# Kernel optimization log

Hardware: AMD Instinct MI355X
Metric: run time of the kernel (lower is better)

Reference implementation:

```python
import jax, jax.numpy as jnp
import numpy as np

N_NODES = 100000
N_EDGES = 1000000
D_NODE = 64
D_EDGE = 32
D_OUT = 64
EPS = 1e-07
BETA = 1.0


def setup_inputs() -> dict:
    key = jax.random.key(0)
    ks = jax.random.split(key, 6)
    node_feats = jax.random.normal(ks[0], (N_NODES, D_NODE), dtype=jnp.float32)
    edge_feats = jax.random.normal(ks[1], (N_EDGES, D_EDGE), dtype=jnp.float32)
    src = jax.random.randint(ks[2], (N_EDGES,), 0, N_NODES, dtype=jnp.int32)
    dst = jax.random.randint(ks[3], (N_EDGES,), 0, N_NODES, dtype=jnp.int32)
    We = jax.random.normal(ks[4], (D_EDGE, D_OUT), dtype=jnp.float32) / np.sqrt(D_EDGE)
    be = jnp.zeros((D_OUT,), dtype=jnp.float32)
    Wm = jax.random.normal(ks[5], (D_NODE, D_OUT), dtype=jnp.float32) / np.sqrt(D_NODE)
    bm = jnp.zeros((D_OUT,), dtype=jnp.float32)
    return {"node_feats": node_feats, "edge_feats": edge_feats, "src": src,
            "dst": dst, "We": We, "be": be, "Wm": Wm, "bm": bm}


def reference(node_feats, edge_feats, src, dst, We, be, Wm, bm):
    n = node_feats.shape[0]
    # edge encoder + u_add_e: m_e = h_src + Linear(e)
    m = node_feats[src] + (edge_feats @ We + be)          # [E, D]
    m = jax.nn.relu(m) + EPS
    # segmented (per-destination) softmax over edges, per feature channel
    z = m * BETA
    zmax = jax.ops.segment_max(z, dst, num_segments=n)    # [N, D]
    ez = jnp.exp(z - zmax[dst])                           # [E, D]
    denom = jax.ops.segment_sum(ez, dst, num_segments=n)  # [N, D]
    a = ez / denom[dst]                                   # [E, D]
    # weighted scatter-sum aggregation
    agg = jax.ops.segment_sum(m * a, dst, num_segments=n) # [N, D]
    feats = node_feats + agg
    # mlp_layers=1 -> single Linear
    return feats @ Wm + bm
```

## Files before the change

### kernel.cpp

```cpp
#include <hip/hip_runtime.h>

#define D_NODE 64
#define D_EDGE 32
#define D_OUT  64
#define EPSF   1e-7f
#define CAP    48
#define CHUNK  8

typedef const __attribute__((address_space(1))) unsigned int guint_t;
typedef __attribute__((address_space(3))) unsigned int luint_t;

__global__ __launch_bounds__(256) void genconv_build_kernel(
    const int* __restrict__ src,
    const int* __restrict__ dst,
    int* __restrict__ cnt,
    int2* __restrict__ slots,
    int E)
{
    const int e = blockIdx.x * blockDim.x + threadIdx.x;
    if (e >= E) return;
    const int d = dst[e];
    const int pos = atomicAdd(&cnt[d], 1);
    if (pos < CAP)
        slots[d * CAP + pos] = make_int2(e, src[e]);
}

__global__ __launch_bounds__(256) void genconv_gather_kernel(
    const float* __restrict__ node,
    const float* __restrict__ ef,
    const int*  __restrict__ cnt,
    const int2* __restrict__ slots,
    const float* __restrict__ We,
    const float* __restrict__ be,
    const float* __restrict__ Wm,
    const float* __restrict__ bm,
    float* __restrict__ out,
    int N)
{
    __shared__ float wm_s[D_NODE * D_OUT];
    __shared__ __align__(16) float efs[4][2][CHUNK * D_EDGE];
    __shared__ __align__(16) float fbuf[4][D_NODE];

    for (int i = threadIdx.x; i < D_NODE * D_OUT; i += blockDim.x)
        wm_s[i] = Wm[i];
    __syncthreads();

    const int lane  = (int)(threadIdx.x & 63);
    const int wslot = (int)(threadIdx.x >> 6);
    float* const efA = efs[wslot][0];
    float* const efB = efs[wslot][1];

    float w[D_EDGE];
#pragma unroll
    for (int k = 0; k < D_EDGE; ++k)
        w[k] = We[k * D_OUT + lane];
    const float bias_e = be[lane];
    const float bias_m = bm[lane];

    const int wid = (int)((blockIdx.x * blockDim.x + threadIdx.x) >> 6);
    const int nw  = (int)((gridDim.x * blockDim.x) >> 6);

    int n = wid;
    int   c_pf   = 0;
    int2  sl_pf  = make_int2(0, 0);
    float res_pf = 0.0f;
    if (n < N) {
        c_pf   = cnt[n];
        sl_pf  = (lane < CAP) ? slots[n * CAP + lane] : make_int2(0, 0);
        res_pf = node[(size_t)n * D_NODE + lane];
    }

    struct HB { float h0, h1, h2, h3, h4, h5, h6, h7; };

    while (n < N) {
        const int c = min(c_pf, CAP);
        const int e_l = (lane < c) ? sl_pf.x : 0;
        const int s_l = (lane < c) ? sl_pf.y : 0;
        const float fres = res_pf;

        const int n_next = n + nw;
        if (n_next < N) {
            c_pf   = cnt[n_next];
            sl_pf  = (lane < CAP) ? slots[n_next * CAP + lane] : make_int2(0, 0);
            res_pf = node[(size_t)n_next * D_NODE + lane];
        }
        __builtin_amdgcn_sched_barrier(0);

        float num = 0.0f, den = 0.0f;

        auto stage = [&](int base, float* dstLDS) {
            const int r  = base + (lane >> 3);
            const int er = __builtin_amdgcn_ds_bpermute(r << 2, e_l);
            const float* g = ef + (size_t)er * D_EDGE + ((lane & 7) << 2);
            __builtin_amdgcn_global_load_lds((guint_t*)g, (luint_t*)dstLDS, 16, 0, 0);
        };
        auto hload = [&](int base, HB& H) {
            const int s0 = __builtin_amdgcn_readlane(s_l, base + 0);
            const int s1 = __builtin_amdgcn_readlane(s_l, base + 1);
            const int s2 = __builtin_amdgcn_readlane(s_l, base + 2);
            const int s3 = __builtin_amdgcn_readlane(s_l, base + 3);
            const int s4 = __builtin_amdgcn_readlane(s_l, base + 4);
            const int s5 = __builtin_amdgcn_readlane(s_l, base + 5);
            const int s6 = __builtin_amdgcn_readlane(s_l, base + 6);
            const int s7 = __builtin_amdgcn_readlane(s_l, base + 7);
            H.h0 = node[(size_t)s0 * D_NODE + lane];
            H.h1 = node[(size_t)s1 * D_NODE + lane];
            H.h2 = node[(size_t)s2 * D_NODE + lane];
            H.h3 = node[(size_t)s3 * D_NODE + lane];
            H.h4 = node[(size_t)s4 * D_NODE + lane];
            H.h5 = node[(size_t)s5 * D_NODE + lane];
            H.h6 = node[(size_t)s6 * D_NODE + lane];
            H.h7 = node[(size_t)s7 * D_NODE + lane];
        };
        auto pairop = [&](float ha, float hb, const float* eb0, bool second_ok) {
            const float* eb1 = eb0 + D_EDGE;
            float v0 = bias_e, v1 = bias_e;
#pragma unroll
            for (int k4 = 0; k4 < 8; ++k4) {
                const float4 a0 = *(const float4*)(eb0 + k4 * 4);
                const float4 a1 = *(const float4*)(eb1 + k4 * 4);
                v0 = fmaf(a0.x, w[4 * k4 + 0], v0);
                v0 = fmaf(a0.y, w[4 * k4 + 1], v0);
                v0 = fmaf(a0.z, w[4 * k4 + 2], v0);
                v0 = fmaf(a0.w, w[4 * k4 + 3], v0);
                v1 = fmaf(a1.x, w[4 * k4 + 0], v1);
                v1 = fmaf(a1.y, w[4 * k4 + 1], v1);
                v1 = fmaf(a1.z, w[4 * k4 + 2], v1);
                v1 = fmaf(a1.w, w[4 * k4 + 3], v1);
            }
            const float m0 = fmaxf(ha + v0, 0.0f) + EPSF;
            const float z0 = __expf(m0);
            num = fmaf(m0, z0, num);
            den += z0;
            if (second_ok) {
                const float m1 = fmaxf(hb + v1, 0.0f) + EPSF;
                const float z1 = __expf(m1);
                num = fmaf(m1, z1, num);
                den += z1;
            }
        };
        auto consume = [&](const float* eb, HB& H, int base) {
            if (base + 0 < c) pairop(H.h0, H.h1, eb + 0 * D_EDGE, base + 1 < c);
            if (base + 2 < c) pairop(H.h2, H.h3, eb + 2 * D_EDGE, base + 3 < c);
            if (base + 4 < c) pairop(H.h4, H.h5, eb + 4 * D_EDGE, base + 5 < c);
            if (base + 6 < c) pairop(H.h6, H.h7, eb + 6 * D_EDGE, base + 7 < c);
        };

        const int nch = (c + CHUNK - 1) >> 3;
        if (nch > 0) {
            HB HA, HB_;
            stage(0, efA);
            hload(0, HA);
            for (int p = 0; ; ) {
                {
                    const bool more = (p + 1 < nch);
                    if (more) { stage((p + 1) * CHUNK, efB); hload((p + 1) * CHUNK, HB_); }
                    if (more) asm volatile("s_waitcnt vmcnt(9)" ::: "memory");
                    else      asm volatile("s_waitcnt vmcnt(0)" ::: "memory");
                    __builtin_amdgcn_sched_barrier(0);
                    consume(efA, HA, p * CHUNK);
                    if (++p >= nch) break;
                }
                {
                    const bool more = (p + 1 < nch);
                    if (more) { stage((p + 1) * CHUNK, efA); hload((p + 1) * CHUNK, HA); }
                    if (more) asm volatile("s_waitcnt vmcnt(9)" ::: "memory");
                    else      asm volatile("s_waitcnt vmcnt(0)" ::: "memory");
                    __builtin_amdgcn_sched_barrier(0);
                    consume(efB, HB_, p * CHUNK);
                    if (++p >= nch) break;
                }
            }
        }

        float f = fres;
        if (c > 0)
            f += num / den;

        fbuf[wslot][lane] = f;
        float acc = bias_m;
#pragma unroll
        for (int d4 = 0; d4 < D_NODE / 4; ++d4) {
            const float4 fv = *(const float4*)&fbuf[wslot][d4 * 4];
            acc = fmaf(fv.x, wm_s[(d4 * 4 + 0) * D_OUT + lane], acc);
            acc = fmaf(fv.y, wm_s[(d4 * 4 + 1) * D_OUT + lane], acc);
            acc = fmaf(fv.z, wm_s[(d4 * 4 + 2) * D_OUT + lane], acc);
            acc = fmaf(fv.w, wm_s[(d4 * 4 + 3) * D_OUT + lane], acc);
        }
        out[(size_t)n * D_NODE + lane] = acc;

        n = n_next;
    }
}

extern "C" void kernel_launch(void* const* d_in, const int* in_sizes, int n_in,
                              void* d_out, int out_size, void* d_ws, size_t ws_size,
                              hipStream_t stream)
{
    const float* node = (const float*)d_in[0];
    const float* ef   = (const float*)d_in[1];
    const int*   src  = (const int*)d_in[2];
    const int*   dst  = (const int*)d_in[3];
    const float* We   = (const float*)d_in[4];
    const float* be   = (const float*)d_in[5];
    const float* Wm   = (const float*)d_in[6];
    const float* bm   = (const float*)d_in[7];
    float* out = (float*)d_out;

    const int N = in_sizes[0] / D_NODE;
    const int E = in_sizes[2];

    int*  cnt   = (int*)d_ws;
    int2* slots = (int2*)(cnt + N);

    hipMemsetAsync(cnt, 0, (size_t)N * sizeof(int), stream);

    genconv_build_kernel<<<(E + 255) / 256, 256, 0, stream>>>(src, dst, cnt, slots, E);

    genconv_gather_kernel<<<2048, 256, 0, stream>>>(node, ef, cnt, slots,
                                                    We, be, Wm, bm, out, N);
}
```

Baseline: 379.2 us.

## Partition destination counters and build slots via histogram, scan, scatter passes

Replaces the single atomic bucket-build with a three-pass scheme: per-partition histograms of destinations, a per-node exclusive scan across partitions, then a scatter using partition-offset atomics. This is intended to spread atomic traffic across eight counter copies. The gather kernel also moves to 512-thread blocks with half the grid. The cost is extra kernel launches, a larger memset and more counter memory traffic.

```diff
diff --git a/kernel.cpp b/kernel.cpp
--- a/kernel.cpp
+++ b/kernel.cpp
@@ -6,26 +6,54 @@
 #define EPSF   1e-7f
 #define CAP    48
 #define CHUNK  8
+#define NPART  8
 
 typedef const __attribute__((address_space(1))) unsigned int guint_t;
 typedef __attribute__((address_space(3))) unsigned int luint_t;
 
-__global__ __launch_bounds__(256) void genconv_build_kernel(
+__global__ __launch_bounds__(256) void genconv_hist_kernel(
+    const int* __restrict__ dst,
+    int* __restrict__ hist,
+    int N, int E)
+{
+    const int e = blockIdx.x * blockDim.x + threadIdx.x;
+    if (e >= E) return;
+    atomicAdd(&hist[(blockIdx.x & (NPART - 1)) * N + dst[e]], 1);
+}
+
+__global__ __launch_bounds__(256) void genconv_scan_kernel(
+    int* __restrict__ hist,
+    int* __restrict__ cnt,
+    int N)
+{
+    const int d = blockIdx.x * blockDim.x + threadIdx.x;
+    if (d >= N) return;
+    int s = 0;
+#pragma unroll
+    for (int x = 0; x < NPART; ++x) {
+        const int t = hist[x * N + d];
+        hist[x * N + d] = s;
+        s += t;
+    }
+    cnt[d] = s;
+}
+
+__global__ __launch_bounds__(256) void genconv_scatter_kernel(
     const int* __restrict__ src,
     const int* __restrict__ dst,
-    int* __restrict__ cnt,
+    int* __restrict__ hist,
     int2* __restrict__ slots,
-    int E)
+    int N, int E)
 {
     const int e = blockIdx.x * blockDim.x + threadIdx.x;
     if (e >= E) return;
     const int d = dst[e];
-    const int pos = atomicAdd(&cnt[d], 1);
+    const int pos = atomicAdd(&hist[(blockIdx.x & (NPART - 1)) * N + d], 1);
     if (pos < CAP)
         slots[d * CAP + pos] = make_int2(e, src[e]);
 }
 
-__global__ __launch_bounds__(256) void genconv_gather_kernel(
+__global__ __launch_bounds__(512) void genconv_gather_kernel(
     const float* __restrict__ node,
     const float* __restrict__ ef,
     const int*  __restrict__ cnt,
@@ -38,8 +66,8 @@
     int N)
 {
     __shared__ float wm_s[D_NODE * D_OUT];
-    __shared__ __align__(16) float efs[4][2][CHUNK * D_EDGE];
-    __shared__ __align__(16) float fbuf[4][D_NODE];
+    __shared__ __align__(16) float efs[8][2][CHUNK * D_EDGE];
+    __shared__ __align__(16) float fbuf[8][D_NODE];
 
     for (int i = threadIdx.x; i < D_NODE * D_OUT; i += blockDim.x)
         wm_s[i] = Wm[i];
@@ -70,7 +98,7 @@
         res_pf = node[(size_t)n * D_NODE + lane];
     }
 
-    struct HB { float h0, h1, h2, h3, h4, h5, h6, h7; };
+    struct HBank { float h0, h1, h2, h3, h4, h5, h6, h7; };
 
     while (n < N) {
         const int c = min(c_pf, CAP);
@@ -94,7 +122,7 @@
             const float* g = ef + (size_t)er * D_EDGE + ((lane & 7) << 2);
             __builtin_amdgcn_global_load_lds((guint_t*)g, (luint_t*)dstLDS, 16, 0, 0);
         };
-        auto hload = [&](int base, HB& H) {
+        auto hload = [&](int base, HBank& H) {
             const int s0 = __builtin_amdgcn_readlane(s_l, base + 0);
             const int s1 = __builtin_amdgcn_readlane(s_l, base + 1);
             const int s2 = __builtin_amdgcn_readlane(s_l, base + 2);
@@ -139,7 +167,7 @@
                 den += z1;
             }
         };
-        auto consume = [&](const float* eb, HB& H, int base) {
+        auto consume = [&](const float* eb, HBank& H, int base) {
             if (base + 0 < c) pairop(H.h0, H.h1, eb + 0 * D_EDGE, base + 1 < c);
             if (base + 2 < c) pairop(H.h2, H.h3, eb + 2 * D_EDGE, base + 3 < c);
             if (base + 4 < c) pairop(H.h4, H.h5, eb + 4 * D_EDGE, base + 5 < c);
@@ -148,7 +176,7 @@
 
         const int nch = (c + CHUNK - 1) >> 3;
         if (nch > 0) {
-            HB HA, HB_;
+            HBank HA, HB_;
             stage(0, efA);
             hload(0, HA);
             for (int p = 0; ; ) {
@@ -211,12 +239,16 @@
     const int E = in_sizes[2];
 
     int*  cnt   = (int*)d_ws;
-    int2* slots = (int2*)(cnt + N);
-
-    hipMemsetAsync(cnt, 0, (size_t)N * sizeof(int), stream);
-
-    genconv_build_kernel<<<(E + 255) / 256, 256, 0, stream>>>(src, dst, cnt, slots, E);
-
-    genconv_gather_kernel<<<2048, 256, 0, stream>>>(node, ef, cnt, slots,
+    int*  hist  = cnt + N;
+    int2* slots = (int2*)(hist + NPART * N);
+
+    hipMemsetAsync(hist, 0, (size_t)NPART * N * sizeof(int), stream);
+
+    const int eblk = (E + 255) / 256;
+    genconv_hist_kernel   <<<eblk, 256, 0, stream>>>(dst, hist, N, E);
+    genconv_scan_kernel   <<<(N + 255) / 256, 256, 0, stream>>>(hist, cnt, N);
+    genconv_scatter_kernel<<<eblk, 256, 0, stream>>>(src, dst, hist, slots, N, E);
+
+    genconv_gather_kernel<<<1024, 512, 0, stream>>>(node, ef, cnt, slots,
                                                     We, be, Wm, bm, out, N);
 }
```

After: 448.5 us. +18.3%, slower.
